# Kernel tuning notes

Hardware: AMD Instinct MI355X
Metric: run time of the kernel (lower is better)

## Reference

```python
import jax, jax.numpy as jnp
import numpy as np

V, D, H, DH, FF, L = 512, 256, 8, 32, 2048, 2
B, S = 4, 128
EPS = 1e-5


def setup_inputs() -> dict:
    key = jax.random.key(0)
    ks = jax.random.split(key, 8)
    rn = lambda k, shape: jax.random.normal(k, shape, jnp.float32) * 0.02
    return {
        "x_t": jax.random.randint(ks[0], (B, S), 0, V),
        "emb": rn(ks[1], (V, D)),
        "temperature": jnp.array(1.0, jnp.float32),
        "Wq": rn(ks[2], (L, D, D)), "Wk": rn(ks[3], (L, D, D)),
        "Wv": rn(ks[4], (L, D, D)), "Wo": rn(ks[5], (L, D, D)),
        "bq": jnp.zeros((L, D)), "bk": jnp.zeros((L, D)),
        "bv": jnp.zeros((L, D)), "bo": jnp.zeros((L, D)),
        "W1": rn(ks[6], (L, D, FF)), "b1": jnp.zeros((L, FF)),
        "W2": rn(ks[7], (L, FF, D)), "b2": jnp.zeros((L, D)),
        "ln1_s": jnp.ones((L, D)), "ln1_b": jnp.zeros((L, D)),
        "ln2_s": jnp.ones((L, D)), "ln2_b": jnp.zeros((L, D)),
    }


def _layer_norm(x, scale, bias):
    m = jnp.mean(x, axis=-1, keepdims=True)
    v = jnp.var(x, axis=-1, keepdims=True)
    return (x - m) / jnp.sqrt(v + EPS) * scale + bias


def reference(x_t, emb, temperature, Wq, Wk, Wv, Wo, bq, bk, bv, bo,
              W1, b1, W2, b2, ln1_s, ln1_b, ln2_s, ln2_b):
    b, s = x_t.shape
    x = emb[x_t]  # [B,S,D]
    scale = 1.0 / np.sqrt(DH).astype(np.float32)
    for l in range(L):  # 2 structurally distinct layers (post-norm, ReLU FFN)
        q = (x @ Wq[l] + bq[l]).reshape(b, s, H, DH)
        k = (x @ Wk[l] + bk[l]).reshape(b, s, H, DH)
        v = (x @ Wv[l] + bv[l]).reshape(b, s, H, DH)
        scores = jnp.einsum('bqhd,bkhd->bhqk', q, k) * scale
        attn = jax.nn.softmax(scores, axis=-1)
        o = jnp.einsum('bhqk,bkhd->bqhd', attn, v).reshape(b, s, D)
        x = _layer_norm(x + (o @ Wo[l] + bo[l]), ln1_s[l], ln1_b[l])
        ff = jax.nn.relu(x @ W1[l] + b1[l]) @ W2[l] + b2[l]
        x = _layer_norm(x + ff, ln2_s[l], ln2_b[l])
    sim = (x @ emb.T) / temperature            # [B,S,V]
    tp = jax.nn.softmax(sim, axis=-1)          # [B,S,V]
    # torch loop `trans_matrix[:,:,i,:] = transition_probs` == broadcast over row dim
    return jnp.broadcast_to(tp[:, :, None, :], (b, s, V, V))
```

## Files before the change

kernel.cpp:

```cpp
#include <hip/hip_runtime.h>
#include <math.h>

#define V_  512
#define D_  256
#define H_  8
#define DH_ 32
#define FF_ 2048
#define L_  2
#define B_  4
#define S_  128
#define T_  (B_*S_)

typedef float f32x4 __attribute__((ext_vector_type(4)));
typedef short s16x8 __attribute__((ext_vector_type(8)));
typedef unsigned short u16x4 __attribute__((ext_vector_type(4)));
typedef unsigned short ushort_t;

__device__ __forceinline__ ushort_t f2b(float f) {
    unsigned int u = __builtin_bit_cast(unsigned int, f);
    u += 0x7FFFu + ((u >> 16) & 1u);
    return (ushort_t)(u >> 16);
}
__device__ __forceinline__ float b2f(ushort_t h) {
    unsigned int u = ((unsigned int)h) << 16;
    return __builtin_bit_cast(float, u);
}

__device__ __forceinline__ float waveReduceSum(float v) {
#pragma unroll
    for (int off = 32; off > 0; off >>= 1) v += __shfl_xor(v, off);
    return v;
}
__device__ __forceinline__ float waveReduceMax(float v) {
#pragma unroll
    for (int off = 32; off > 0; off >>= 1) v = fmaxf(v, __shfl_xor(v, off));
    return v;
}

template<int RELU, int OUTB, int BIAS>
__device__ __forceinline__ void mgemm_body(
    const ushort_t* __restrict__ A, const ushort_t* __restrict__ BT,
    const float* __restrict__ bias, float* __restrict__ Cf,
    ushort_t* __restrict__ Cb, int M, int N, int K, int kBegin, int kSteps)
{
    __shared__ ushort_t Al[2][64][72];
    __shared__ ushort_t Bl[2][64][72];
    const int tid  = threadIdx.x;
    const int m0   = blockIdx.y * 64, n0 = blockIdx.x * 64;
    const int lane = tid & 63, w = tid >> 6;
    const int srow = tid >> 2, sseg = (tid & 3) * 16;
    const int l15  = lane & 15,  kg = (lane >> 4) * 8;

    f32x4 acc0 = {0.f,0.f,0.f,0.f}, acc1 = acc0, acc2 = acc0, acc3 = acc0;

    const ushort_t* Aptr = &A [(size_t)(m0 + srow) * K + kBegin + sseg];
    const ushort_t* Bptr = &BT[(size_t)(n0 + srow) * K + kBegin + sseg];

    s16x8 av0 = *(const s16x8*)Aptr,       av1 = *(const s16x8*)(Aptr + 8);
    s16x8 bv0 = *(const s16x8*)Bptr,       bv1 = *(const s16x8*)(Bptr + 8);
    *(s16x8*)&Al[0][srow][sseg]     = av0;
    *(s16x8*)&Al[0][srow][sseg + 8] = av1;
    *(s16x8*)&Bl[0][srow][sseg]     = bv0;
    *(s16x8*)&Bl[0][srow][sseg + 8] = bv1;

    for (int kt = 0; kt < kSteps; ++kt) {
        const int cur = kt & 1;
        const bool more = (kt + 1 < kSteps);
        if (more) {
            const size_t o = (size_t)(kt + 1) * 64;
            av0 = *(const s16x8*)(Aptr + o);     av1 = *(const s16x8*)(Aptr + o + 8);
            bv0 = *(const s16x8*)(Bptr + o);     bv1 = *(const s16x8*)(Bptr + o + 8);
        }
        asm volatile("s_waitcnt lgkmcnt(0)\n\ts_barrier" ::: "memory");

        s16x8 b0 = *(const s16x8*)&Bl[cur][w * 16 + l15][kg];
        s16x8 b1 = *(const s16x8*)&Bl[cur][w * 16 + l15][kg + 32];
        s16x8 a00 = *(const s16x8*)&Al[cur][     l15][kg];
        s16x8 a01 = *(const s16x8*)&Al[cur][     l15][kg + 32];
        s16x8 a10 = *(const s16x8*)&Al[cur][16 + l15][kg];
        s16x8 a11 = *(const s16x8*)&Al[cur][16 + l15][kg + 32];
        s16x8 a20 = *(const s16x8*)&Al[cur][32 + l15][kg];
        s16x8 a21 = *(const s16x8*)&Al[cur][32 + l15][kg + 32];
        s16x8 a30 = *(const s16x8*)&Al[cur][48 + l15][kg];
        s16x8 a31 = *(const s16x8*)&Al[cur][48 + l15][kg + 32];
        acc0 = __builtin_amdgcn_mfma_f32_16x16x32_bf16(a00, b0, acc0, 0, 0, 0);
        acc1 = __builtin_amdgcn_mfma_f32_16x16x32_bf16(a10, b0, acc1, 0, 0, 0);
        acc2 = __builtin_amdgcn_mfma_f32_16x16x32_bf16(a20, b0, acc2, 0, 0, 0);
        acc3 = __builtin_amdgcn_mfma_f32_16x16x32_bf16(a30, b0, acc3, 0, 0, 0);
        acc0 = __builtin_amdgcn_mfma_f32_16x16x32_bf16(a01, b1, acc0, 0, 0, 0);
        acc1 = __builtin_amdgcn_mfma_f32_16x16x32_bf16(a11, b1, acc1, 0, 0, 0);
        acc2 = __builtin_amdgcn_mfma_f32_16x16x32_bf16(a21, b1, acc2, 0, 0, 0);
        acc3 = __builtin_amdgcn_mfma_f32_16x16x32_bf16(a31, b1, acc3, 0, 0, 0);

        if (more) {
            *(s16x8*)&Al[cur ^ 1][srow][sseg]     = av0;
            *(s16x8*)&Al[cur ^ 1][srow][sseg + 8] = av1;
            *(s16x8*)&Bl[cur ^ 1][srow][sseg]     = bv0;
            *(s16x8*)&Bl[cur ^ 1][srow][sseg + 8] = bv1;
        }
    }

    const int col = n0 + w * 16 + l15;
    const float bb = BIAS ? bias[col] : 0.f;
    f32x4 accs[4] = {acc0, acc1, acc2, acc3};
#pragma unroll
    for (int r = 0; r < 4; ++r) {
#pragma unroll
        for (int e = 0; e < 4; ++e) {
            const int row = m0 + r * 16 + (lane >> 4) * 4 + e;
            float v = accs[r][e] + bb;
            if (RELU) v = fmaxf(v, 0.f);
            if (OUTB) Cb[(size_t)row * N + col] = f2b(v);
            else      Cf[(size_t)row * N + col] = v;
        }
    }
}

template<int RELU, int OUTB, int BIAS>
__global__ __launch_bounds__(256) void mgemm_k(const ushort_t* A, const ushort_t* BT,
    const float* bias, float* Cf0, float* Cf1, ushort_t* Cb,
    int M, int N, int K, int kChunk)
{
    const int z = blockIdx.z;
    float* Cfz = nullptr;
    if (Cf0) Cfz = (z < 2) ? Cf0 + (size_t)z * M * N
                           : Cf1 + (size_t)(z - 2) * M * N;
    mgemm_body<RELU, OUTB, BIAS>(A, BT, bias, Cfz, Cb, M, N, K,
                                 z * kChunk, kChunk / 64);
}

__global__ __launch_bounds__(256) void qkv_k(const ushort_t* Xb, const ushort_t* WT,
    const float* bq, const float* bk, const float* bv,
    ushort_t* Qb, ushort_t* Kb, ushort_t* Vb)
{
    const int z = blockIdx.z;
    const ushort_t* bt = WT + (size_t)z * (D_ * D_);
    const float* bias; ushort_t* out;
    if (z == 0)      { bias = bq; out = Qb; }
    else if (z == 1) { bias = bk; out = Kb; }
    else             { bias = bv; out = Vb; }
    mgemm_body<0, 1, 1>(Xb, bt, bias, nullptr, out, T_, D_, D_, 0, D_ / 64);
}

__global__ __launch_bounds__(256) void prep_k(const int* __restrict__ xt,
    const float* __restrict__ emb, float* __restrict__ X,
    ushort_t* __restrict__ Xb, ushort_t* __restrict__ embB,
    const float* __restrict__ Wq, const float* __restrict__ Wk,
    const float* __restrict__ Wv, const float* __restrict__ Wo,
    const float* __restrict__ W1, const float* __restrict__ W2,
    ushort_t* __restrict__ WT, ushort_t* __restrict__ W1T, ushort_t* __restrict__ W2T)
{
    __shared__ float Tl[32][33];
    const int tid = threadIdx.x;
    if (blockIdx.x < 512) {
        const int idx = blockIdx.x * 256 + tid;
        const int t = idx >> 8, d = idx & 255;
        const float v = emb[(size_t)xt[t] * D_ + d];
        X[idx]  = v;
        Xb[idx] = f2b(v);
        embB[idx] = f2b(emb[idx]);
        return;
    }
    const int id = blockIdx.x - 512;
    const int l  = id >= 1280 ? 1 : 0;
    const int t  = id - l * 1280;
    const float* src; ushort_t* dst; int R, C, rt, ct;
    if (t < 256) {
        const int kind = t >> 6, tl = t & 63;
        const float* s0 = (kind == 0) ? Wq : (kind == 1) ? Wk : (kind == 2) ? Wv : Wo;
        src = s0 + (size_t)l * (D_ * D_);
        dst = WT + (size_t)l * (4 * D_ * D_) + (size_t)kind * (D_ * D_);
        R = D_; C = D_; rt = tl >> 3; ct = tl & 7;
    } else if (t < 768) {
        const int tl = t - 256;
        src = W1 + (size_t)l * (D_ * FF_); dst = W1T + (size_t)l * (D_ * FF_);
        R = D_; C = FF_; rt = tl >> 6; ct = tl & 63;
    } else {
        const int tl = t - 768;
        src = W2 + (size_t)l * (FF_ * D_); dst = W2T + (size_t)l * (FF_ * D_);
        R = FF_; C = D_; rt = tl >> 3; ct = tl & 7;
    }
    const int r = tid >> 3, c4 = (tid & 7) * 4;
    f32x4 v = *(const f32x4*)&src[(size_t)(rt * 32 + r) * C + ct * 32 + c4];
    Tl[r][c4] = v[0]; Tl[r][c4 + 1] = v[1]; Tl[r][c4 + 2] = v[2]; Tl[r][c4 + 3] = v[3];
    __syncthreads();
    u16x4 ov;
    ov[0] = f2b(Tl[c4 + 0][r]); ov[1] = f2b(Tl[c4 + 1][r]);
    ov[2] = f2b(Tl[c4 + 2][r]); ov[3] = f2b(Tl[c4 + 3][r]);
    *(u16x4*)&dst[(size_t)(ct * 32 + r) * R + rt * 32 + c4] = ov;
}

__global__ __launch_bounds__(256) void add_ln_k(
    const float* __restrict__ p0, const float* __restrict__ p1, int nparts,
    const float* __restrict__ bias, float* __restrict__ X,
    ushort_t* __restrict__ Xb, const float* __restrict__ s,
    const float* __restrict__ b)
{
    __shared__ float red[4];
    const int row = blockIdx.x, tid = threadIdx.x;
    const size_t off = (size_t)row * D_ + tid;
    const size_t TD = (size_t)T_ * D_;
    float a = X[off] + bias[tid] + p0[off];
    if (nparts >= 2) a += p0[TD + off];
    if (nparts == 4) a += p1[off] + p1[TD + off];

    float ws_ = waveReduceSum(a);
    if ((tid & 63) == 0) red[tid >> 6] = ws_;
    __syncthreads();
    const float mean = (red[0] + red[1] + red[2] + red[3]) * (1.f / D_);
    __syncthreads();
    const float d = a - mean;
    float vs = waveReduceSum(d * d);
    if ((tid & 63) == 0) red[tid >> 6] = vs;
    __syncthreads();
    const float var = (red[0] + red[1] + red[2] + red[3]) * (1.f / D_);
    const float y = d * rsqrtf(var + 1e-5f) * s[tid] + b[tid];
    X[off]  = y;
    Xb[off] = f2b(y);
}

__global__ __launch_bounds__(256) void attn_k(const ushort_t* __restrict__ Qb,
    const ushort_t* __restrict__ Kb, const ushort_t* __restrict__ Vb,
    ushort_t* __restrict__ Ob)
{
    __shared__ float Qs[32][36], Ks[128][36], Vs[128][36], Ps[32][132];
    const int bh = blockIdx.x, b = bh >> 3, h = bh & 7;
    const int i0 = blockIdx.y * 32;
    const int tid = threadIdx.x;

#pragma unroll
    for (int it = 0; it < 2; ++it) {
        const int g = it * 256 + tid;
        const int r = g >> 2, c8 = (g & 3) * 8;
        s16x8 kv = *(const s16x8*)&Kb[(size_t)(b * S_ + r) * D_ + h * DH_ + c8];
        s16x8 vv = *(const s16x8*)&Vb[(size_t)(b * S_ + r) * D_ + h * DH_ + c8];
        f32x4 klo = {b2f((ushort_t)kv[0]), b2f((ushort_t)kv[1]), b2f((ushort_t)kv[2]), b2f((ushort_t)kv[3])};
        f32x4 khi = {b2f((ushort_t)kv[4]), b2f((ushort_t)kv[5]), b2f((ushort_t)kv[6]), b2f((ushort_t)kv[7])};
        f32x4 vlo = {b2f((ushort_t)vv[0]), b2f((ushort_t)vv[1]), b2f((ushort_t)vv[2]), b2f((ushort_t)vv[3])};
        f32x4 vhi = {b2f((ushort_t)vv[4]), b2f((ushort_t)vv[5]), b2f((ushort_t)vv[6]), b2f((ushort_t)vv[7])};
        *(f32x4*)&Ks[r][c8]     = klo;  *(f32x4*)&Ks[r][c8 + 4] = khi;
        *(f32x4*)&Vs[r][c8]     = vlo;  *(f32x4*)&Vs[r][c8 + 4] = vhi;
    }
    if (tid < 128) {
        const int r = tid >> 2, c8 = (tid & 3) * 8;
        s16x8 qv = *(const s16x8*)&Qb[(size_t)(b * S_ + i0 + r) * D_ + h * DH_ + c8];
        f32x4 qlo = {b2f((ushort_t)qv[0]), b2f((ushort_t)qv[1]), b2f((ushort_t)qv[2]), b2f((ushort_t)qv[3])};
        f32x4 qhi = {b2f((ushort_t)qv[4]), b2f((ushort_t)qv[5]), b2f((ushort_t)qv[6]), b2f((ushort_t)qv[7])};
        *(f32x4*)&Qs[r][c8] = qlo;  *(f32x4*)&Qs[r][c8 + 4] = qhi;
    }
    __syncthreads();

    const int i = tid >> 3, jg = tid & 7;
    const float sc = 0.17677669529663687f;
    float sv[16];
    float mx = -1e30f;
#pragma unroll
    for (int jj = 0; jj < 16; ++jj) {
        const int j = jg + jj * 8;
        f32x4 a4 = {0.f,0.f,0.f,0.f};
#pragma unroll
        for (int kk = 0; kk < 8; ++kk) {
            f32x4 q = *(const f32x4*)&Qs[i][kk * 4];
            f32x4 k = *(const f32x4*)&Ks[j][kk * 4];
            a4 += q * k;
        }
        const float sdot = (a4[0] + a4[1] + a4[2] + a4[3]) * sc;
        sv[jj] = sdot;
        mx = fmaxf(mx, sdot);
    }
    mx = fmaxf(mx, __shfl_xor(mx, 1));
    mx = fmaxf(mx, __shfl_xor(mx, 2));
    mx = fmaxf(mx, __shfl_xor(mx, 4));
    float sum = 0.f;
#pragma unroll
    for (int jj = 0; jj < 16; ++jj) {
        const float e = __expf(sv[jj] - mx);
        Ps[i][jg + jj * 8] = e;
        sum += e;
    }
    sum += __shfl_xor(sum, 1);
    sum += __shfl_xor(sum, 2);
    sum += __shfl_xor(sum, 4);
    const float inv = 1.f / sum;
    __syncthreads();

    const int dg = tid & 7;
    f32x4 o = {0.f,0.f,0.f,0.f};
#pragma unroll 4
    for (int j = 0; j < 128; ++j) {
        const float p = Ps[i][j];
        f32x4 vv = *(const f32x4*)&Vs[j][dg * 4];
        o += vv * p;
    }
    u16x4 ov;
    ov[0] = f2b(o[0] * inv); ov[1] = f2b(o[1] * inv);
    ov[2] = f2b(o[2] * inv); ov[3] = f2b(o[3] * inv);
    *(u16x4*)&Ob[(size_t)(b * S_ + i0 + i) * D_ + h * DH_ + dg * 4] = ov;
}

__global__ __launch_bounds__(256) void bcast_k(const float* __restrict__ Lg,
    const float* __restrict__ temp, float* __restrict__ out)
{
    __shared__ float row[V_];
    __shared__ float red[4];
    const int blk = blockIdx.x, t = blk >> 2, quarter = blk & 3;
    const int tid = threadIdx.x;
    const float rT = 1.f / temp[0];
    const float l0 = Lg[(size_t)t * V_ + tid] * rT;
    const float l1 = Lg[(size_t)t * V_ + 256 + tid] * rT;
    float m = waveReduceMax(fmaxf(l0, l1));
    if ((tid & 63) == 0) red[tid >> 6] = m;
    __syncthreads();
    m = fmaxf(fmaxf(red[0], red[1]), fmaxf(red[2], red[3]));
    __syncthreads();
    const float e0 = __expf(l0 - m), e1 = __expf(l1 - m);
    float sblk = waveReduceSum(e0 + e1);
    if ((tid & 63) == 0) red[tid >> 6] = sblk;
    __syncthreads();
    const float inv = 1.f / (red[0] + red[1] + red[2] + red[3]);
    row[tid] = e0 * inv;
    row[tid + 256] = e1 * inv;
    __syncthreads();

    const int c = tid & 127, ihalf = tid >> 7;
    f32x4 v = *(const f32x4*)&row[c * 4];
    f32x4* dst = (f32x4*)out + (size_t)t * V_ * (V_ / 4);
#pragma unroll 4
    for (int r = 0; r < 64; ++r) {
        const int i = quarter * 128 + ihalf + r * 2;
        __builtin_nontemporal_store(v, &dst[(size_t)i * (V_ / 4) + c]);
    }
}

extern "C" void kernel_launch(void* const* d_in, const int* in_sizes, int n_in,
                              void* d_out, int out_size, void* d_ws, size_t ws_size,
                              hipStream_t stream)
{
    const int*   x_t  = (const int*)  d_in[0];
    const float* emb  = (const float*)d_in[1];
    const float* temp = (const float*)d_in[2];
    const float* Wq   = (const float*)d_in[3];
    const float* Wk   = (const float*)d_in[4];
    const float* Wv   = (const float*)d_in[5];
    const float* Wo   = (const float*)d_in[6];
    const float* bq   = (const float*)d_in[7];
    const float* bk   = (const float*)d_in[8];
    const float* bv   = (const float*)d_in[9];
    const float* bo   = (const float*)d_in[10];
    const float* W1   = (const float*)d_in[11];
    const float* b1   = (const float*)d_in[12];
    const float* W2   = (const float*)d_in[13];
    const float* b2   = (const float*)d_in[14];
    const float* ln1s = (const float*)d_in[15];
    const float* ln1b = (const float*)d_in[16];
    const float* ln2s = (const float*)d_in[17];
    const float* ln2b = (const float*)d_in[18];

    float* out = (float*)d_out;
    char*  wsb = (char*)d_ws;

    float*    X     = (float*)   (wsb + 0);
    float*    PartA = (float*)   (wsb + 524288);
    float*    Lg    = PartA;
    ushort_t* Qb    = (ushort_t*)(wsb + 1572864);
    float*    PartB = (float*)   (wsb + 1572864);
    ushort_t* Kb    = (ushort_t*)(wsb + 1835008);
    ushort_t* Vb    = (ushort_t*)(wsb + 2097152);
    ushort_t* Ob    = (ushort_t*)(wsb + 2359296);
    ushort_t* Xb    = (ushort_t*)(wsb + 2621440);
    ushort_t* Ffb   = (ushort_t*)(wsb + 2883584);
    ushort_t* embB  = (ushort_t*)(wsb + 4980736);
    ushort_t* WT    = (ushort_t*)(wsb + 5242880);
    ushort_t* W1T   = (ushort_t*)(wsb + 6291456);
    ushort_t* W2T   = (ushort_t*)(wsb + 8388608);

    prep_k<<<3072, 256, 0, stream>>>(x_t, emb, X, Xb, embB,
                                     Wq, Wk, Wv, Wo, W1, W2, WT, W1T, W2T);

    for (int l = 0; l < L_; ++l) {
        const ushort_t* WTl  = WT  + (size_t)l * (4 * D_ * D_);
        const ushort_t* W1Tl = W1T + (size_t)l * (D_ * FF_);
        const ushort_t* W2Tl = W2T + (size_t)l * (FF_ * D_);

        qkv_k<<<dim3(4, 8, 3), 256, 0, stream>>>(
            Xb, WTl, bq + l * D_, bk + l * D_, bv + l * D_, Qb, Kb, Vb);

        attn_k<<<dim3(32, 4), 256, 0, stream>>>(Qb, Kb, Vb, Ob);

        mgemm_k<0, 0, 0><<<dim3(4, 8, 2), 256, 0, stream>>>(
            Ob, WTl + 3 * D_ * D_, nullptr, PartA, nullptr, nullptr,
            T_, D_, D_, D_ / 2);
        add_ln_k<<<T_, 256, 0, stream>>>(PartA, nullptr, 2, bo + l * D_,
                                         X, Xb, ln1s + l * D_, ln1b + l * D_);

        mgemm_k<1, 1, 1><<<dim3(32, 8, 1), 256, 0, stream>>>(
            Xb, W1Tl, b1 + l * FF_, nullptr, nullptr, Ffb, T_, FF_, D_, D_);

        mgemm_k<0, 0, 0><<<dim3(4, 8, 4), 256, 0, stream>>>(
            Ffb, W2Tl, nullptr, PartA, PartB, nullptr, T_, D_, FF_, FF_ / 4);
        add_ln_k<<<T_, 256, 0, stream>>>(PartA, PartB, 4, b2 + l * D_,
                                         X, Xb, ln2s + l * D_, ln2b + l * D_);
    }

    mgemm_k<0, 0, 0><<<dim3(8, 8, 1), 256, 0, stream>>>(
        Xb, embB, nullptr, Lg, nullptr, nullptr, T_, V_, D_, D_);

    bcast_k<<<T_ * 4, 256, 0, stream>>>(Lg, temp, out);
}
```

Before: 172.6 us.

## Fuse QKV projection into attention kernel, computing per-head Q/K/V in registers

Replaces the separate QKV GEMM kernel and attention kernel with a single kernel where each (batch, head, query-block) block computes its head's K and V for all 128 keys and Q for its 32 queries via MFMA, writing fp32 directly into shared memory. This removes one kernel launch per layer and the bf16 round-trip of Q/K/V through global memory. The cost is that K/V projections are recomputed redundantly by the 4 query-block tiles of each head, and operands are loaded straight from global memory without LDS staging. Q/K/V also stay in fp32 rather than being rounded to bf16.

```diff
diff --git a/kernel.cpp b/kernel.cpp
--- a/kernel.cpp
+++ b/kernel.cpp
@@ -73,8 +73,8 @@
         }
         asm volatile("s_waitcnt lgkmcnt(0)\n\ts_barrier" ::: "memory");
 
-        s16x8 b0 = *(const s16x8*)&Bl[cur][w * 16 + l15][kg];
-        s16x8 b1 = *(const s16x8*)&Bl[cur][w * 16 + l15][kg + 32];
+        s16x8 b0  = *(const s16x8*)&Bl[cur][w * 16 + l15][kg];
+        s16x8 b1  = *(const s16x8*)&Bl[cur][w * 16 + l15][kg + 32];
         s16x8 a00 = *(const s16x8*)&Al[cur][     l15][kg];
         s16x8 a01 = *(const s16x8*)&Al[cur][     l15][kg + 32];
         s16x8 a10 = *(const s16x8*)&Al[cur][16 + l15][kg];
@@ -129,17 +129,123 @@
                                  z * kChunk, kChunk / 64);
 }
 
-__global__ __launch_bounds__(256) void qkv_k(const ushort_t* Xb, const ushort_t* WT,
-    const float* bq, const float* bk, const float* bv,
-    ushort_t* Qb, ushort_t* Kb, ushort_t* Vb)
-{
-    const int z = blockIdx.z;
-    const ushort_t* bt = WT + (size_t)z * (D_ * D_);
-    const float* bias; ushort_t* out;
-    if (z == 0)      { bias = bq; out = Qb; }
-    else if (z == 1) { bias = bk; out = Kb; }
-    else             { bias = bv; out = Vb; }
-    mgemm_body<0, 1, 1>(Xb, bt, bias, nullptr, out, T_, D_, D_, 0, D_ / 64);
+__global__ __launch_bounds__(256) void qkvattn_k(
+    const ushort_t* __restrict__ Xb, const ushort_t* __restrict__ WT,
+    const float* __restrict__ bq, const float* __restrict__ bk,
+    const float* __restrict__ bv, ushort_t* __restrict__ Ob)
+{
+    __shared__ float Qs[32][36], Ks[128][36], Vs[128][36], Ps[32][132];
+    const int bh = blockIdx.x, b = bh >> 3, h = bh & 7;
+    const int i0 = blockIdx.y * 32;
+    const int tid = threadIdx.x;
+    const int w = tid >> 6, lane = tid & 63;
+    const int l15 = lane & 15, kg = (lane >> 4) * 8;
+
+    {
+        const ushort_t* WqT = WT + (size_t)(h * DH_) * D_;
+        const ushort_t* WkT = WqT + (size_t)D_ * D_;
+        const ushort_t* WvT = WqT + 2 * (size_t)D_ * D_;
+        const ushort_t* Akv = Xb + (size_t)(b * S_ + w * 32) * D_;
+        const int qmf = w >> 1, qnf = w & 1;
+        const ushort_t* Aq  = Xb + (size_t)(b * S_ + i0 + qmf * 16) * D_;
+
+        f32x4 kacc00 = {0.f,0.f,0.f,0.f}, kacc01 = kacc00, kacc10 = kacc00, kacc11 = kacc00;
+        f32x4 vacc00 = kacc00, vacc01 = kacc00, vacc10 = kacc00, vacc11 = kacc00;
+        f32x4 qacc = kacc00;
+#pragma unroll
+        for (int kk = 0; kk < 8; ++kk) {
+            const int k0 = kk * 32 + kg;
+            s16x8 a0  = *(const s16x8*)&Akv[(size_t)(     l15) * D_ + k0];
+            s16x8 a1  = *(const s16x8*)&Akv[(size_t)(16 + l15) * D_ + k0];
+            s16x8 aq  = *(const s16x8*)&Aq [(size_t)(     l15) * D_ + k0];
+            s16x8 wk0 = *(const s16x8*)&WkT[(size_t)(     l15) * D_ + k0];
+            s16x8 wk1 = *(const s16x8*)&WkT[(size_t)(16 + l15) * D_ + k0];
+            s16x8 wv0 = *(const s16x8*)&WvT[(size_t)(     l15) * D_ + k0];
+            s16x8 wv1 = *(const s16x8*)&WvT[(size_t)(16 + l15) * D_ + k0];
+            s16x8 wq  = *(const s16x8*)&WqT[(size_t)(qnf * 16 + l15) * D_ + k0];
+            kacc00 = __builtin_amdgcn_mfma_f32_16x16x32_bf16(a0, wk0, kacc00, 0, 0, 0);
+            kacc01 = __builtin_amdgcn_mfma_f32_16x16x32_bf16(a0, wk1, kacc01, 0, 0, 0);
+            kacc10 = __builtin_amdgcn_mfma_f32_16x16x32_bf16(a1, wk0, kacc10, 0, 0, 0);
+            kacc11 = __builtin_amdgcn_mfma_f32_16x16x32_bf16(a1, wk1, kacc11, 0, 0, 0);
+            vacc00 = __builtin_amdgcn_mfma_f32_16x16x32_bf16(a0, wv0, vacc00, 0, 0, 0);
+            vacc01 = __builtin_amdgcn_mfma_f32_16x16x32_bf16(a0, wv1, vacc01, 0, 0, 0);
+            vacc10 = __builtin_amdgcn_mfma_f32_16x16x32_bf16(a1, wv0, vacc10, 0, 0, 0);
+            vacc11 = __builtin_amdgcn_mfma_f32_16x16x32_bf16(a1, wv1, vacc11, 0, 0, 0);
+            qacc   = __builtin_amdgcn_mfma_f32_16x16x32_bf16(aq, wq,  qacc,   0, 0, 0);
+        }
+        const int r0 = (lane >> 4) * 4;
+        f32x4 kaccs[2][2] = {{kacc00, kacc01}, {kacc10, kacc11}};
+        f32x4 vaccs[2][2] = {{vacc00, vacc01}, {vacc10, vacc11}};
+#pragma unroll
+        for (int mf = 0; mf < 2; ++mf) {
+#pragma unroll
+            for (int nf = 0; nf < 2; ++nf) {
+                const int col = nf * 16 + l15;
+                const float kb = bk[h * DH_ + col];
+                const float vb = bv[h * DH_ + col];
+#pragma unroll
+                for (int e = 0; e < 4; ++e) {
+                    Ks[w * 32 + mf * 16 + r0 + e][col] = kaccs[mf][nf][e] + kb;
+                    Vs[w * 32 + mf * 16 + r0 + e][col] = vaccs[mf][nf][e] + vb;
+                }
+            }
+        }
+        {
+            const int col = qnf * 16 + l15;
+            const float qb = bq[h * DH_ + col];
+#pragma unroll
+            for (int e = 0; e < 4; ++e)
+                Qs[qmf * 16 + r0 + e][col] = qacc[e] + qb;
+        }
+    }
+    __syncthreads();
+
+    const int i = tid >> 3, jg = tid & 7;
+    const float sc = 0.17677669529663687f;
+    float sv[16];
+    float mx = -1e30f;
+#pragma unroll
+    for (int jj = 0; jj < 16; ++jj) {
+        const int j = jg + jj * 8;
+        f32x4 a4 = {0.f,0.f,0.f,0.f};
+#pragma unroll
+        for (int kk = 0; kk < 8; ++kk) {
+            f32x4 q = *(const f32x4*)&Qs[i][kk * 4];
+            f32x4 k = *(const f32x4*)&Ks[j][kk * 4];
+            a4 += q * k;
+        }
+        const float sdot = (a4[0] + a4[1] + a4[2] + a4[3]) * sc;
+        sv[jj] = sdot;
+        mx = fmaxf(mx, sdot);
+    }
+    mx = fmaxf(mx, __shfl_xor(mx, 1));
+    mx = fmaxf(mx, __shfl_xor(mx, 2));
+    mx = fmaxf(mx, __shfl_xor(mx, 4));
+    float sum = 0.f;
+#pragma unroll
+    for (int jj = 0; jj < 16; ++jj) {
+        const float e = __expf(sv[jj] - mx);
+        Ps[i][jg + jj * 8] = e;
+        sum += e;
+    }
+    sum += __shfl_xor(sum, 1);
+    sum += __shfl_xor(sum, 2);
+    sum += __shfl_xor(sum, 4);
+    const float inv = 1.f / sum;
+    __syncthreads();
+
+    const int dg = tid & 7;
+    f32x4 o = {0.f,0.f,0.f,0.f};
+#pragma unroll 4
+    for (int j = 0; j < 128; ++j) {
+        const float p = Ps[i][j];
+        f32x4 vv = *(const f32x4*)&Vs[j][dg * 4];
+        o += vv * p;
+    }
+    u16x4 ov;
+    ov[0] = f2b(o[0] * inv); ov[1] = f2b(o[1] * inv);
+    ov[2] = f2b(o[2] * inv); ov[3] = f2b(o[3] * inv);
+    *(u16x4*)&Ob[(size_t)(b * S_ + i0 + i) * D_ + h * DH_ + dg * 4] = ov;
 }
 
 __global__ __launch_bounds__(256) void prep_k(const int* __restrict__ xt,
@@ -217,85 +323,6 @@
     const float y = d * rsqrtf(var + 1e-5f) * s[tid] + b[tid];
     X[off]  = y;
     Xb[off] = f2b(y);
-}
-
-__global__ __launch_bounds__(256) void attn_k(const ushort_t* __restrict__ Qb,
-    const ushort_t* __restrict__ Kb, const ushort_t* __restrict__ Vb,
-    ushort_t* __restrict__ Ob)
-{
-    __shared__ float Qs[32][36], Ks[128][36], Vs[128][36], Ps[32][132];
-    const int bh = blockIdx.x, b = bh >> 3, h = bh & 7;
-    const int i0 = blockIdx.y * 32;
-    const int tid = threadIdx.x;
-
-#pragma unroll
-    for (int it = 0; it < 2; ++it) {
-        const int g = it * 256 + tid;
-        const int r = g >> 2, c8 = (g & 3) * 8;
-        s16x8 kv = *(const s16x8*)&Kb[(size_t)(b * S_ + r) * D_ + h * DH_ + c8];
-        s16x8 vv = *(const s16x8*)&Vb[(size_t)(b * S_ + r) * D_ + h * DH_ + c8];
-        f32x4 klo = {b2f((ushort_t)kv[0]), b2f((ushort_t)kv[1]), b2f((ushort_t)kv[2]), b2f((ushort_t)kv[3])};
-        f32x4 khi = {b2f((ushort_t)kv[4]), b2f((ushort_t)kv[5]), b2f((ushort_t)kv[6]), b2f((ushort_t)kv[7])};
-        f32x4 vlo = {b2f((ushort_t)vv[0]), b2f((ushort_t)vv[1]), b2f((ushort_t)vv[2]), b2f((ushort_t)vv[3])};
-        f32x4 vhi = {b2f((ushort_t)vv[4]), b2f((ushort_t)vv[5]), b2f((ushort_t)vv[6]), b2f((ushort_t)vv[7])};
-        *(f32x4*)&Ks[r][c8]     = klo;  *(f32x4*)&Ks[r][c8 + 4] = khi;
-        *(f32x4*)&Vs[r][c8]     = vlo;  *(f32x4*)&Vs[r][c8 + 4] = vhi;
-    }
-    if (tid < 128) {
-        const int r = tid >> 2, c8 = (tid & 3) * 8;
-        s16x8 qv = *(const s16x8*)&Qb[(size_t)(b * S_ + i0 + r) * D_ + h * DH_ + c8];
-        f32x4 qlo = {b2f((ushort_t)qv[0]), b2f((ushort_t)qv[1]), b2f((ushort_t)qv[2]), b2f((ushort_t)qv[3])};
-        f32x4 qhi = {b2f((ushort_t)qv[4]), b2f((ushort_t)qv[5]), b2f((ushort_t)qv[6]), b2f((ushort_t)qv[7])};
-        *(f32x4*)&Qs[r][c8] = qlo;  *(f32x4*)&Qs[r][c8 + 4] = qhi;
-    }
-    __syncthreads();
-
-    const int i = tid >> 3, jg = tid & 7;
-    const float sc = 0.17677669529663687f;
-    float sv[16];
-    float mx = -1e30f;
-#pragma unroll
-    for (int jj = 0; jj < 16; ++jj) {
-        const int j = jg + jj * 8;
-        f32x4 a4 = {0.f,0.f,0.f,0.f};
-#pragma unroll
-        for (int kk = 0; kk < 8; ++kk) {
-            f32x4 q = *(const f32x4*)&Qs[i][kk * 4];
-            f32x4 k = *(const f32x4*)&Ks[j][kk * 4];
-            a4 += q * k;
-        }
-        const float sdot = (a4[0] + a4[1] + a4[2] + a4[3]) * sc;
-        sv[jj] = sdot;
-        mx = fmaxf(mx, sdot);
-    }
-    mx = fmaxf(mx, __shfl_xor(mx, 1));
-    mx = fmaxf(mx, __shfl_xor(mx, 2));
-    mx = fmaxf(mx, __shfl_xor(mx, 4));
-    float sum = 0.f;
-#pragma unroll
-    for (int jj = 0; jj < 16; ++jj) {
-        const float e = __expf(sv[jj] - mx);
-        Ps[i][jg + jj * 8] = e;
-        sum += e;
-    }
-    sum += __shfl_xor(sum, 1);
-    sum += __shfl_xor(sum, 2);
-    sum += __shfl_xor(sum, 4);
-    const float inv = 1.f / sum;
-    __syncthreads();
-
-    const int dg = tid & 7;
-    f32x4 o = {0.f,0.f,0.f,0.f};
-#pragma unroll 4
-    for (int j = 0; j < 128; ++j) {
-        const float p = Ps[i][j];
-        f32x4 vv = *(const f32x4*)&Vs[j][dg * 4];
-        o += vv * p;
-    }
-    u16x4 ov;
-    ov[0] = f2b(o[0] * inv); ov[1] = f2b(o[1] * inv);
-    ov[2] = f2b(o[2] * inv); ov[3] = f2b(o[3] * inv);
-    *(u16x4*)&Ob[(size_t)(b * S_ + i0 + i) * D_ + h * DH_ + dg * 4] = ov;
 }
 
 __global__ __launch_bounds__(256) void bcast_k(const float* __restrict__ Lg,
@@ -362,10 +389,7 @@
     float*    X     = (float*)   (wsb + 0);
     float*    PartA = (float*)   (wsb + 524288);
     float*    Lg    = PartA;
-    ushort_t* Qb    = (ushort_t*)(wsb + 1572864);
     float*    PartB = (float*)   (wsb + 1572864);
-    ushort_t* Kb    = (ushort_t*)(wsb + 1835008);
-    ushort_t* Vb    = (ushort_t*)(wsb + 2097152);
     ushort_t* Ob    = (ushort_t*)(wsb + 2359296);
     ushort_t* Xb    = (ushort_t*)(wsb + 2621440);
     ushort_t* Ffb   = (ushort_t*)(wsb + 2883584);
@@ -382,10 +406,8 @@
         const ushort_t* W1Tl = W1T + (size_t)l * (D_ * FF_);
         const ushort_t* W2Tl = W2T + (size_t)l * (FF_ * D_);
 
-        qkv_k<<<dim3(4, 8, 3), 256, 0, stream>>>(
-            Xb, WTl, bq + l * D_, bk + l * D_, bv + l * D_, Qb, Kb, Vb);
-
-        attn_k<<<dim3(32, 4), 256, 0, stream>>>(Qb, Kb, Vb, Ob);
+        qkvattn_k<<<dim3(32, 4), 256, 0, stream>>>(
+            Xb, WTl, bq + l * D_, bk + l * D_, bv + l * D_, Ob);
 
         mgemm_k<0, 0, 0><<<dim3(4, 8, 2), 256, 0, stream>>>(
             Ob, WTl + 3 * D_ * D_, nullptr, PartA, nullptr, nullptr,
```

New measurement: 178.0 us. +3.1%, slower.
